# Optimization experiments

Hardware: AMD Instinct MI355X
Metric: run time of the kernel (lower is better)

Reference implementation:

```python
import jax, jax.numpy as jnp
import numpy as np

H, W, N = 1024, 2048, 1572864
NF, NP, NIN = 32, 3, 5


def _linear_init(key, fan_in, fan_out):
    kw, kb = jax.random.split(key)
    bound = 1.0 / np.sqrt(fan_in)
    w = jax.random.uniform(kw, (fan_in, fan_out), jnp.float32, -bound, bound)
    b = jax.random.uniform(kb, (fan_out,), jnp.float32, -bound, bound)
    return w, b


def setup_inputs() -> dict:
    key = jax.random.key(0)
    ks = jax.random.split(key, 8)
    # grid: sub-pixel source coordinates, (2, N), x-row then y-row
    gx = jax.random.uniform(ks[0], (1, N), jnp.float32) * (W - 1)
    gy = jax.random.uniform(ks[1], (1, N), jnp.float32) * (H - 1)
    grid = jnp.concatenate([gx, gy], axis=0)
    # yi: unique flat pixel indices (torch index-assign assumes no duplicates)
    yi = jax.random.permutation(ks[2], H * W)[:N].astype(jnp.int32)
    # m: near-identity homography so the projective denominator stays well-conditioned
    m = jnp.eye(3, dtype=jnp.float32) + 0.05 * jax.random.normal(ks[3], (3, 3), jnp.float32)
    W1, b1 = _linear_init(ks[4], NIN, NF)
    W2, b2 = _linear_init(ks[5], NF, NF)
    W3, b3 = _linear_init(ks[6], NF, NF)
    W4, b4 = _linear_init(ks[7], NF, NP)
    return {"grid": grid, "yi": yi, "m": m,
            "W1": W1, "b1": b1, "W2": W2, "b2": b2,
            "W3": W3, "b3": b3, "W4": W4, "b4": b4,
            "size_h": H, "size_w": W}


def _calc_dsda_projective(m, h, w):
    # Area scale (Jacobian determinant magnitude) of the homography m at each
    # output pixel: |det(m)| / |m20*x + m21*y + m22|^3, flattened row-major (H*W,)
    xs = jnp.arange(w, dtype=jnp.float32)
    ys = jnp.arange(h, dtype=jnp.float32)
    denom = m[2, 0] * xs[None, :] + m[2, 1] * ys[:, None] + m[2, 2]  # (H, W)
    det = jnp.linalg.det(m)
    return (jnp.abs(det) / (jnp.abs(denom) ** 3)).reshape(-1)


def reference(grid, yi, m, W1, b1, W2, b2, W3, b3, W4, b4, size_h, size_w):
    h, w = size_h, size_w
    # --- feature construction (torch.no_grad block) ---
    dsda = _calc_dsda_projective(m, h, w)[yi][:, None]          # (N, 1) gather
    g = grid.T                                                  # (N, 2)
    gf = jnp.floor(g)
    tl = g - gf                                                 # x-fx, y-fy
    br = 1.0 - tl                                               # fx+1-x, fy+1-y
    x = jax.lax.stop_gradient(jnp.concatenate([tl, br, dsda], axis=1))  # (N, 5)
    # --- tiny 4-layer MLP ---
    hdd = jax.nn.relu(x @ W1 + b1)
    hdd = jax.nn.relu(hdd @ W2 + b2)
    hdd = jax.nn.relu(hdd @ W3 + b3)
    logits = hdd @ W4 + b4                                      # (N, NP)
    wgt = jax.nn.softmax(logits, axis=1)
    # --- scatter back to spatial layout ---
    w_spatial = jnp.zeros((h * w, NP), dtype=wgt.dtype).at[yi].set(wgt)
    return w_spatial.reshape(1, 1, h, w, NP)
```

## Files before the change

### kernel.cpp

```cpp
#include <hip/hip_runtime.h>


#define W_IMG 2048

typedef __attribute__((ext_vector_type(8)))  _Float16 f16x8;
typedef __attribute__((ext_vector_type(16))) float    f32x16;
typedef __attribute__((ext_vector_type(2)))  __fp16   h16x2;

union DWu { h16x2 h; unsigned u; };
union B8u { f16x8 v; unsigned u[4]; };

__device__ __forceinline__ void l32swap(unsigned &x, unsigned &y) {
#if __has_builtin(__builtin_amdgcn_permlane32_swap)
    auto r = __builtin_amdgcn_permlane32_swap(x, y, false, false);
    x = (unsigned)r[0];
    y = (unsigned)r[1];
#else
    unsigned sx = (unsigned)__shfl_xor((int)x, 32, 64);
    unsigned sy = (unsigned)__shfl_xor((int)y, 32, 64);
    bool up = (threadIdx.x & 32) != 0;
    unsigned nx = up ? sy : x;
    unsigned ny = up ? y  : sx;
    x = nx; y = ny;
#endif
}

__device__ __forceinline__ unsigned pkrc(float a, float b) {
    a = fminf(fmaxf(a, 0.f), 60000.f);
    b = fminf(fmaxf(b, 0.f), 60000.f);
    DWu d; d.h = __builtin_amdgcn_cvt_pkrtz(a, b);
    return d.u;
}

__global__ __launch_bounds__(256) void fill_zero(float* __restrict__ out, int n) {
    int n4 = n >> 2;
    float4* o4 = (float4*)out;
    int stride = gridDim.x * blockDim.x;
    for (int i = blockIdx.x * blockDim.x + threadIdx.x; i < n4; i += stride)
        o4[i] = make_float4(0.f, 0.f, 0.f, 0.f);
    int t = (n4 << 2) + (blockIdx.x * blockDim.x + threadIdx.x);
    if (t < n) out[t] = 0.f;
}

__global__ __launch_bounds__(256, 4) void msampler_mlp(
    const float* __restrict__ grid,
    const int*   __restrict__ yi,
    const float* __restrict__ m,
    const float* __restrict__ W1, const float* __restrict__ b1,
    const float* __restrict__ W2, const float* __restrict__ b2,
    const float* __restrict__ W3, const float* __restrict__ b3,
    const float* __restrict__ W4, const float* __restrict__ b4,
    float* __restrict__ out, int N)
{
    const int tid  = threadIdx.x;
    const int lane = tid & 63;
    const int wave = tid >> 6;
    const int m32  = lane & 31;
    const int h    = lane >> 5;

    B8u a1;
#pragma unroll
    for (int j = 0; j < 8; ++j) {
        int k = 8*h + j;
        float w = 0.f;
        if (h == 0) {
            if (k < 5)       w = W1[k*32 + m32];
            else if (k == 5) w = b1[m32];
        }
        a1.v[j] = (_Float16)w;
    }
    B8u a2[2], a3[2], a4[2];
#pragma unroll
    for (int q = 0; q < 2; ++q) {
#pragma unroll
        for (int j = 0; j < 8; ++j) {
            int k = q*16 + 8*h + j;
            a2[q].v[j] = (_Float16)W2[k*32 + m32];
            a3[q].v[j] = (_Float16)W3[k*32 + m32];
            a4[q].v[j] = (m32 < 3) ? (_Float16)W4[k*3 + m32] : (_Float16)0.f;
        }
    }
    f32x16 cb2, cb3;
#pragma unroll
    for (int r = 0; r < 16; ++r) {
        int row = (r & 3) + 8*(r >> 2) + 4*h;
        cb2[r] = b2[row];
        cb3[r] = b3[row];
    }
    const float B40 = b4[0], B41 = b4[1], B42 = b4[2];

    float m20 = m[6], m21 = m[7], m22 = m[8];
    float det = m[0]*(m[4]*m22 - m[5]*m21)
              - m[1]*(m[3]*m22 - m[5]*m20)
              + m[2]*(m[3]*m21 - m[4]*m20);
    float adet = fabsf(det);

    const int i0 = blockIdx.x * 512 + wave * 128;
    int ya[2];
    unsigned fdw[2][3];
#pragma unroll
    for (int p = 0; p < 2; ++p) {
        int i  = i0 + p*64 + lane;
        int ic = i < N ? i : N - 1;
        float gx = grid[ic];
        float gy = grid[N + ic];
        int   y  = yi[ic];
        ya[p] = y;
        int py = y >> 11;
        int px = y & (W_IMG - 1);
        float denom = m20*(float)px + m21*(float)py + m22;
        float ad    = fabsf(denom);
        float dsda  = fminf(adet / (ad*ad*ad), 60000.f);
        float fx = gx - floorf(gx);
        float fy = gy - floorf(gy);
        DWu d0; d0.h = __builtin_amdgcn_cvt_pkrtz(fx, fy);
        DWu d1; d1.h = __builtin_amdgcn_cvt_pkrtz(1.f - fx, 1.f - fy);
        DWu d2; d2.h = __builtin_amdgcn_cvt_pkrtz(dsda, 1.f);
        fdw[p][0] = d0.u; fdw[p][1] = d1.u; fdw[p][2] = d2.u;
    }

    float lg[2][3];
    unsigned dw[8];

#define PACKSWAP(ACC, BA, BB)                                                 \
    {                                                                         \
        _Pragma("unroll")                                                     \
        for (int r2 = 0; r2 < 8; ++r2)                                        \
            dw[r2] = pkrc(ACC[2*r2], ACC[2*r2+1]);                            \
        l32swap(dw[0], dw[2]); l32swap(dw[1], dw[3]);                         \
        l32swap(dw[4], dw[6]); l32swap(dw[5], dw[7]);                         \
        BA.u[0]=dw[0]; BA.u[1]=dw[1]; BA.u[2]=dw[2]; BA.u[3]=dw[3];           \
        BB.u[0]=dw[4]; BB.u[1]=dw[5]; BB.u[2]=dw[6]; BB.u[3]=dw[7];           \
    }

#pragma unroll
    for (int t = 0; t < 4; ++t) {
        const int  p     = t >> 1;
        const bool upper = (t & 1) != 0;

        B8u bf;
        if (!upper) {
            bf.u[0] = fdw[p][0]; bf.u[1] = fdw[p][1];
            bf.u[2] = fdw[p][2]; bf.u[3] = 0u;
        } else {
            unsigned x0 = fdw[p][0], y0 = 0u; l32swap(x0, y0);
            unsigned x1 = fdw[p][1], y1 = 0u; l32swap(x1, y1);
            unsigned x2 = fdw[p][2], y2 = 0u; l32swap(x2, y2);
            bf.u[0] = y0; bf.u[1] = y1; bf.u[2] = y2; bf.u[3] = 0u;
        }

        f32x16 acc;
#pragma unroll
        for (int r = 0; r < 16; ++r) acc[r] = 0.f;
        acc = __builtin_amdgcn_mfma_f32_32x32x16_f16(a1.v, bf.v, acc, 0, 0, 0);

        B8u bA, bB;
        PACKSWAP(acc, bA, bB)

        acc = __builtin_amdgcn_mfma_f32_32x32x16_f16(a2[0].v, bA.v, cb2, 0, 0, 0);
        acc = __builtin_amdgcn_mfma_f32_32x32x16_f16(a2[1].v, bB.v, acc, 0, 0, 0);
        PACKSWAP(acc, bA, bB)

        acc = __builtin_amdgcn_mfma_f32_32x32x16_f16(a3[0].v, bA.v, cb3, 0, 0, 0);
        acc = __builtin_amdgcn_mfma_f32_32x32x16_f16(a3[1].v, bB.v, acc, 0, 0, 0);
        PACKSWAP(acc, bA, bB)

        f32x16 acc4;
#pragma unroll
        for (int r = 0; r < 16; ++r) acc4[r] = 0.f;
        acc4 = __builtin_amdgcn_mfma_f32_32x32x16_f16(a4[0].v, bA.v, acc4, 0, 0, 0);
        acc4 = __builtin_amdgcn_mfma_f32_32x32x16_f16(a4[1].v, bB.v, acc4, 0, 0, 0);

        if (!upper) {
            lg[p][0] = acc4[0]; lg[p][1] = acc4[1]; lg[p][2] = acc4[2];
        } else {
            unsigned g0 = __float_as_uint(acc4[0]), d0 = 0u; l32swap(d0, g0);
            unsigned g1 = __float_as_uint(acc4[1]), d1 = 0u; l32swap(d1, g1);
            unsigned g2 = __float_as_uint(acc4[2]), d2 = 0u; l32swap(d2, g2);
            if (lane >= 32) {
                lg[p][0] = __uint_as_float(d0);
                lg[p][1] = __uint_as_float(d1);
                lg[p][2] = __uint_as_float(d2);
            }
        }
    }
#undef PACKSWAP

#pragma unroll
    for (int p = 0; p < 2; ++p) {
        float l0 = lg[p][0] + B40;
        float l1 = lg[p][1] + B41;
        float l2 = lg[p][2] + B42;
        float mx = fmaxf(l0, fmaxf(l1, l2));
        float e0 = __expf(l0 - mx), e1 = __expf(l1 - mx), e2 = __expf(l2 - mx);
        float inv = 1.f / (e0 + e1 + e2);
        int i = i0 + p*64 + lane;
        if (i < N) {
            int o = ya[p] * 3;
            out[o + 0] = e0 * inv;
            out[o + 1] = e1 * inv;
            out[o + 2] = e2 * inv;
        }
    }
}

extern "C" void kernel_launch(void* const* d_in, const int* in_sizes, int n_in,
                              void* d_out, int out_size, void* d_ws, size_t ws_size,
                              hipStream_t stream) {
    const float* grid = (const float*)d_in[0];
    const int*   yi   = (const int*)  d_in[1];
    const float* m    = (const float*)d_in[2];
    const float* W1   = (const float*)d_in[3];
    const float* b1   = (const float*)d_in[4];
    const float* W2   = (const float*)d_in[5];
    const float* b2   = (const float*)d_in[6];
    const float* W3   = (const float*)d_in[7];
    const float* b3   = (const float*)d_in[8];
    const float* W4   = (const float*)d_in[9];
    const float* b4   = (const float*)d_in[10];
    float* out = (float*)d_out;

    int N = in_sizes[1];

    fill_zero<<<2048, 256, 0, stream>>>(out, out_size);

    int grid_sz = (N + 511) / 512;
    msampler_mlp<<<grid_sz, 256, 0, stream>>>(
        grid, yi, m, W1, b1, W2, b2, W3, b3, W4, b4, out, N);
}
```

Before: 136.9 us.

## Map points to lower half-wave lanes to drop cross-half swaps in MLP

Feature construction, softmax and the scatter store now run only in lanes 0-31, and each of the four MFMA tiles takes 32 points directly. This removes the permlane32 swaps that moved inputs and logits between wave halves. The fallback swap becomes inline asm, the zero accumulator is hoisted, and the occupancy hint drops from 4 to 3 waves. In exchange, the elementwise front and the stores use only half of each wave, which halves lane utilisation for the memory gathers and scatters.

```diff
diff --git a/kernel.cpp b/kernel.cpp
--- a/kernel.cpp
+++ b/kernel.cpp
@@ -16,12 +16,7 @@
     x = (unsigned)r[0];
     y = (unsigned)r[1];
 #else
-    unsigned sx = (unsigned)__shfl_xor((int)x, 32, 64);
-    unsigned sy = (unsigned)__shfl_xor((int)y, 32, 64);
-    bool up = (threadIdx.x & 32) != 0;
-    unsigned nx = up ? sy : x;
-    unsigned ny = up ? y  : sx;
-    x = nx; y = ny;
+    asm volatile("v_permlane32_swap_b32 %0, %1" : "+v"(x), "+v"(y));
 #endif
 }
 
@@ -42,7 +37,7 @@
     if (t < n) out[t] = 0.f;
 }
 
-__global__ __launch_bounds__(256, 4) void msampler_mlp(
+__global__ __launch_bounds__(256, 3) void msampler_mlp(
     const float* __restrict__ grid,
     const int*   __restrict__ yi,
     const float* __restrict__ m,
@@ -80,12 +75,13 @@
             a4[q].v[j] = (m32 < 3) ? (_Float16)W4[k*3 + m32] : (_Float16)0.f;
         }
     }
-    f32x16 cb2, cb3;
+    f32x16 cb2, cb3, zacc;
 #pragma unroll
     for (int r = 0; r < 16; ++r) {
         int row = (r & 3) + 8*(r >> 2) + 4*h;
         cb2[r] = b2[row];
         cb3[r] = b3[row];
+        zacc[r] = 0.f;
     }
     const float B40 = b4[0], B41 = b4[1], B42 = b4[2];
 
@@ -96,63 +92,58 @@
     float adet = fabsf(det);
 
     const int i0 = blockIdx.x * 512 + wave * 128;
-    int ya[2];
-    unsigned fdw[2][3];
-#pragma unroll
-    for (int p = 0; p < 2; ++p) {
-        int i  = i0 + p*64 + lane;
-        int ic = i < N ? i : N - 1;
-        float gx = grid[ic];
-        float gy = grid[N + ic];
-        int   y  = yi[ic];
-        ya[p] = y;
-        int py = y >> 11;
-        int px = y & (W_IMG - 1);
-        float denom = m20*(float)px + m21*(float)py + m22;
-        float ad    = fabsf(denom);
-        float dsda  = fminf(adet / (ad*ad*ad), 60000.f);
-        float fx = gx - floorf(gx);
-        float fy = gy - floorf(gy);
-        DWu d0; d0.h = __builtin_amdgcn_cvt_pkrtz(fx, fy);
-        DWu d1; d1.h = __builtin_amdgcn_cvt_pkrtz(1.f - fx, 1.f - fy);
-        DWu d2; d2.h = __builtin_amdgcn_cvt_pkrtz(dsda, 1.f);
-        fdw[p][0] = d0.u; fdw[p][1] = d1.u; fdw[p][2] = d2.u;
-    }
-
-    float lg[2][3];
-    unsigned dw[8];
+    int ya[4];
+    unsigned fdw[4][3];
+    if (lane < 32) {
+#pragma unroll
+        for (int t = 0; t < 4; ++t) {
+            int i  = i0 + t*32 + m32;
+            int ic = i < N ? i : N - 1;
+            float gx = grid[ic];
+            float gy = grid[N + ic];
+            int   y  = yi[ic];
+            ya[t] = y;
+            int py = y >> 11;
+            int px = y & (W_IMG - 1);
+            float denom = m20*(float)px + m21*(float)py + m22;
+            float ad    = fabsf(denom);
+            float dsda  = fminf(adet / (ad*ad*ad), 60000.f);
+            float fx = gx - floorf(gx);
+            float fy = gy - floorf(gy);
+            DWu d0; d0.h = __builtin_amdgcn_cvt_pkrtz(fx, fy);
+            DWu d1; d1.h = __builtin_amdgcn_cvt_pkrtz(1.f - fx, 1.f - fy);
+            DWu d2; d2.h = __builtin_amdgcn_cvt_pkrtz(dsda, 1.f);
+            fdw[t][0] = d0.u; fdw[t][1] = d1.u; fdw[t][2] = d2.u;
+        }
+    }
+
+    float lg[4][3];
 
 #define PACKSWAP(ACC, BA, BB)                                                 \
     {                                                                         \
-        _Pragma("unroll")                                                     \
-        for (int r2 = 0; r2 < 8; ++r2)                                        \
-            dw[r2] = pkrc(ACC[2*r2], ACC[2*r2+1]);                            \
-        l32swap(dw[0], dw[2]); l32swap(dw[1], dw[3]);                         \
-        l32swap(dw[4], dw[6]); l32swap(dw[5], dw[7]);                         \
-        BA.u[0]=dw[0]; BA.u[1]=dw[1]; BA.u[2]=dw[2]; BA.u[3]=dw[3];           \
-        BB.u[0]=dw[4]; BB.u[1]=dw[5]; BB.u[2]=dw[6]; BB.u[3]=dw[7];           \
+        unsigned dw0 = pkrc(ACC[0],  ACC[1]);                                 \
+        unsigned dw1 = pkrc(ACC[2],  ACC[3]);                                 \
+        unsigned dw2 = pkrc(ACC[4],  ACC[5]);                                 \
+        unsigned dw3 = pkrc(ACC[6],  ACC[7]);                                 \
+        unsigned dw4 = pkrc(ACC[8],  ACC[9]);                                 \
+        unsigned dw5 = pkrc(ACC[10], ACC[11]);                                \
+        unsigned dw6 = pkrc(ACC[12], ACC[13]);                                \
+        unsigned dw7 = pkrc(ACC[14], ACC[15]);                                \
+        l32swap(dw0, dw2); l32swap(dw1, dw3);                                 \
+        l32swap(dw4, dw6); l32swap(dw5, dw7);                                 \
+        BA.u[0]=dw0; BA.u[1]=dw1; BA.u[2]=dw2; BA.u[3]=dw3;                   \
+        BB.u[0]=dw4; BB.u[1]=dw5; BB.u[2]=dw6; BB.u[3]=dw7;                   \
     }
 
 #pragma unroll
     for (int t = 0; t < 4; ++t) {
-        const int  p     = t >> 1;
-        const bool upper = (t & 1) != 0;
-
         B8u bf;
-        if (!upper) {
-            bf.u[0] = fdw[p][0]; bf.u[1] = fdw[p][1];
-            bf.u[2] = fdw[p][2]; bf.u[3] = 0u;
-        } else {
-            unsigned x0 = fdw[p][0], y0 = 0u; l32swap(x0, y0);
-            unsigned x1 = fdw[p][1], y1 = 0u; l32swap(x1, y1);
-            unsigned x2 = fdw[p][2], y2 = 0u; l32swap(x2, y2);
-            bf.u[0] = y0; bf.u[1] = y1; bf.u[2] = y2; bf.u[3] = 0u;
-        }
-
-        f32x16 acc;
-#pragma unroll
-        for (int r = 0; r < 16; ++r) acc[r] = 0.f;
-        acc = __builtin_amdgcn_mfma_f32_32x32x16_f16(a1.v, bf.v, acc, 0, 0, 0);
+        bf.u[0] = (h == 0) ? fdw[t][0] : 0u;
+        bf.u[1] = (h == 0) ? fdw[t][1] : 0u;
+        bf.u[2] = (h == 0) ? fdw[t][2] : 0u;
+        bf.u[3] = 0u;
+
+        f32x16 acc = __builtin_amdgcn_mfma_f32_32x32x16_f16(a1.v, bf.v, zacc, 0, 0, 0);
 
         B8u bA, bB;
         PACKSWAP(acc, bA, bB)
@@ -165,41 +156,28 @@
         acc = __builtin_amdgcn_mfma_f32_32x32x16_f16(a3[1].v, bB.v, acc, 0, 0, 0);
         PACKSWAP(acc, bA, bB)
 
-        f32x16 acc4;
-#pragma unroll
-        for (int r = 0; r < 16; ++r) acc4[r] = 0.f;
-        acc4 = __builtin_amdgcn_mfma_f32_32x32x16_f16(a4[0].v, bA.v, acc4, 0, 0, 0);
+        f32x16 acc4 = __builtin_amdgcn_mfma_f32_32x32x16_f16(a4[0].v, bA.v, zacc, 0, 0, 0);
         acc4 = __builtin_amdgcn_mfma_f32_32x32x16_f16(a4[1].v, bB.v, acc4, 0, 0, 0);
-
-        if (!upper) {
-            lg[p][0] = acc4[0]; lg[p][1] = acc4[1]; lg[p][2] = acc4[2];
-        } else {
-            unsigned g0 = __float_as_uint(acc4[0]), d0 = 0u; l32swap(d0, g0);
-            unsigned g1 = __float_as_uint(acc4[1]), d1 = 0u; l32swap(d1, g1);
-            unsigned g2 = __float_as_uint(acc4[2]), d2 = 0u; l32swap(d2, g2);
-            if (lane >= 32) {
-                lg[p][0] = __uint_as_float(d0);
-                lg[p][1] = __uint_as_float(d1);
-                lg[p][2] = __uint_as_float(d2);
+        lg[t][0] = acc4[0]; lg[t][1] = acc4[1]; lg[t][2] = acc4[2];
+    }
+#undef PACKSWAP
+
+    if (lane < 32) {
+#pragma unroll
+        for (int t = 0; t < 4; ++t) {
+            float l0 = lg[t][0] + B40;
+            float l1 = lg[t][1] + B41;
+            float l2 = lg[t][2] + B42;
+            float mx = fmaxf(l0, fmaxf(l1, l2));
+            float e0 = __expf(l0 - mx), e1 = __expf(l1 - mx), e2 = __expf(l2 - mx);
+            float inv = 1.f / (e0 + e1 + e2);
+            int i = i0 + t*32 + m32;
+            if (i < N) {
+                int o = ya[t] * 3;
+                out[o + 0] = e0 * inv;
+                out[o + 1] = e1 * inv;
+                out[o + 2] = e2 * inv;
             }
-        }
-    }
-#undef PACKSWAP
-
-#pragma unroll
-    for (int p = 0; p < 2; ++p) {
-        float l0 = lg[p][0] + B40;
-        float l1 = lg[p][1] + B41;
-        float l2 = lg[p][2] + B42;
-        float mx = fmaxf(l0, fmaxf(l1, l2));
-        float e0 = __expf(l0 - mx), e1 = __expf(l1 - mx), e2 = __expf(l2 - mx);
-        float inv = 1.f / (e0 + e1 + e2);
-        int i = i0 + p*64 + lane;
-        if (i < N) {
-            int o = ya[p] * 3;
-            out[o + 0] = e0 * inv;
-            out[o + 1] = e1 * inv;
-            out[o + 2] = e2 * inv;
         }
     }
 }
```

Measured after the change: 137.5 us. No clear change (+0.4%).
